# Performance work log

Hardware: AMD Instinct MI355X
Metric: run time of the kernel (lower is better)

The kernel has to match this reference:

```python
import jax, jax.numpy as jnp
import numpy as np

D_HID = 512
N_HEADS = 16
D_HEAD = D_HID // N_HEADS  # 32
D_FFN = 2048
B, N = 4, 1024
FACTOR = 0.5 / np.sqrt(D_HEAD)
EPS = 1e-5


def layer_norm(x, g, b):
    m = x.mean(-1, keepdims=True)
    v = ((x - m) ** 2).mean(-1, keepdims=True)
    return (x - m) / jnp.sqrt(v + EPS) * g + b


def setup_inputs() -> dict:
    key = jax.random.key(0)
    ks = jax.random.split(key, 24)
    s = 0.02
    p = lambda k, shape: jax.random.normal(k, shape, jnp.float32) * s
    inp = {
        'H': jax.random.normal(ks[0], (B, N, D_HID), jnp.float32),
        'V': jax.random.normal(ks[1], (B, N, 3, D_HID), jnp.float32),
        'D_batch': jax.random.normal(ks[2], (B, N, N), jnp.float32),
        'rbf_bias': jax.random.normal(ks[3], (B, 1, N, N), jnp.float32),
        'H_mask': jax.random.randint(ks[4], (B, N), 0, 2, jnp.int32),
        # attention sublayer params
        'g1': jnp.ones((D_HID,), jnp.float32), 'beta1': jnp.zeros((D_HID,), jnp.float32),
        'Wq': p(ks[5], (D_HID, 4 * D_HID)), 'bq': p(ks[6], (4 * D_HID,)),
        'Wk': p(ks[7], (D_HID, 4 * D_HID)), 'bk': p(ks[8], (4 * D_HID,)),
        'Wv': p(ks[9], (D_HID, D_HID)), 'bv': p(ks[10], (D_HID,)),
        'Wvv': p(ks[11], (D_HID, D_HID)),
        'Wo': p(ks[12], (D_HID, D_HID)), 'bo': p(ks[13], (D_HID,)),
        'Wvo': p(ks[14], (D_HID, D_HID)),
        # GVP FFN sublayer params
        'g2': jnp.ones((D_HID,), jnp.float32), 'beta2': jnp.zeros((D_HID,), jnp.float32),
        'Wlv': p(ks[15], (D_HID, 2 * D_HID)),
        'W1': p(ks[16], (2 * D_HID, D_FFN)), 'b1f': p(ks[17], (D_FFN,)),
        'W2': p(ks[18], (D_FFN, 2 * D_HID)), 'b2f': p(ks[19], (2 * D_HID,)),
    }
    return inp


def ept_forward(H, V, D_batch, rbf_bias, H_mask, g1, beta1, Wq, bq, Wk, bk, Wv, bv,
                Wvv, Wo, bo, Wvo, g2, beta2, Wlv, W1, b1f, W2, b2f):
    b, n, d = H.shape
    # ---- attention sublayer (pre-LN on H only, residual on H and V) ----
    Hn = layer_norm(H, g1, beta1)
    Hq = (Hn @ Wq + bq).reshape(b, n, N_HEADS, 4 * D_HEAD)
    Hk = (Hn @ Wk + bk).reshape(b, n, N_HEADS, 4 * D_HEAD)
    Hv = (Hn @ Wv + bv).reshape(b, n, N_HEADS, D_HEAD)
    # vector values: [b,n,3,d] -> [b,n,heads,3*dh]
    Vv = (V @ Wvv).reshape(b, n, 3, N_HEADS, D_HEAD).transpose(0, 1, 3, 2, 4)
    Vv = Vv.reshape(b, n, N_HEADS, 3 * D_HEAD)
    V_attn = jnp.concatenate([Hv, Vv], axis=-1)  # [b,n,h,4*dh]
    bias = rbf_bias + D_batch[:, None]  # [b,1,n,n]
    keep = (H_mask != 0)[:, None, None, :]  # mask keys
    bias = jnp.where(keep, bias, -jnp.inf)
    logits = jnp.einsum('bnhd,bmhd->bhnm', Hq, Hk) * FACTOR + bias
    attn = jax.nn.softmax(logits, axis=-1)
    res = jnp.einsum('bhnm,bmhd->bnhd', attn, V_attn)  # [b,n,h,4*dh]
    H_res = res[..., :D_HEAD].reshape(b, n, d)
    V_res = res[..., D_HEAD:].reshape(b, n, N_HEADS, 3, D_HEAD)
    V_res = V_res.transpose(0, 1, 3, 2, 4).reshape(b, n, 3, d)
    H = H + H_res @ Wo + bo
    V = V + V_res @ Wvo
    # ---- GVP FFN sublayer (pre-LN on H only, residual) ----
    Hn2 = layer_norm(H, g2, beta2)
    Vp = V @ Wlv  # [b,n,3,2d]
    V1, V2 = Vp[..., :d], Vp[..., d:]
    scaler = jnp.concatenate([Hn2, jnp.sqrt((V1 ** 2).sum(axis=-2))], axis=-1)
    h = jax.nn.silu(scaler @ W1 + b1f) @ W2 + b2f  # [b,n,2d]
    H = H + h[..., :d]
    V = V + h[..., None, d:] * V2
    return H, V


def reference(H, V, D_batch, rbf_bias, H_mask, g1, beta1, Wq, bq, Wk, bk, Wv, bv,
              Wvv, Wo, bo, Wvo, g2, beta2, Wlv, W1, b1f, W2, b2f):
    return ept_forward(H, V, D_batch, rbf_bias, H_mask, g1, beta1, Wq, bq, Wk, bk,
                       Wv, bv, Wvv, Wo, bo, Wvo, g2, beta2, Wlv, W1, b1f, W2, b2f)
```

## Files before the change

kernel.cpp:

```cpp
#include <hip/hip_runtime.h>
#include <math.h>

#define NBATCH 4
#define NSEQ   1024
#define DHID   512
#define NHEADS 16
#define ROWS   (NBATCH*NSEQ)
#define VROWS  (ROWS*3)
#define ATT_FACTOR 0.08838834764831845f
#define LOG2E 1.4426950408889634f
#define F2 (ATT_FACTOR*LOG2E)
#define SM_SHIFT (16.0f*LOG2E)

typedef __attribute__((ext_vector_type(8))) short short8;
typedef __attribute__((ext_vector_type(4))) float floatx4;

__device__ __forceinline__ ushort f2bf(float x) {
  union { float f; unsigned u; } v; v.f = x;
  unsigned r = v.u + 0x7fff + ((v.u >> 16) & 1);
  return (ushort)(r >> 16);
}
__device__ __forceinline__ float bf2f(ushort u) {
  union { unsigned u; float f; } v; v.u = ((unsigned)u) << 16; return v.f;
}

template<int OBF>
__global__ __launch_bounds__(256) void ln_kernel(
    const float* __restrict__ x, void* __restrict__ y, int ystride,
    const float* __restrict__ g, const float* __restrict__ beta)
{
  int row = blockIdx.x;
  int t = threadIdx.x;
  const float* xr = x + (size_t)row * DHID;
  float2 v = ((const float2*)xr)[t];
  float s  = v.x + v.y;
  float ss = v.x*v.x + v.y*v.y;
  #pragma unroll
  for (int off = 32; off > 0; off >>= 1) {
    s  += __shfl_down(s, off);
    ss += __shfl_down(ss, off);
  }
  __shared__ float red[8];
  int w = t >> 6;
  if ((t & 63) == 0) { red[w*2] = s; red[w*2+1] = ss; }
  __syncthreads();
  s  = red[0] + red[2] + red[4] + red[6];
  ss = red[1] + red[3] + red[5] + red[7];
  float mean = s * (1.0f/DHID);
  float var  = ss * (1.0f/DHID) - mean*mean;
  float rstd = rsqrtf(var + 1e-5f);
  float2 gg = ((const float2*)g)[t];
  float2 bb = ((const float2*)beta)[t];
  float2 o;
  o.x = (v.x - mean) * rstd * gg.x + bb.x;
  o.y = (v.y - mean) * rstd * gg.y + bb.y;
  if constexpr (OBF) {
    ushort2 u = { f2bf(o.x), f2bf(o.y) };
    *(ushort2*)&((ushort*)y)[(size_t)row * ystride + 2*t] = u;
  } else {
    *(float2*)&((float*)y)[(size_t)row * ystride + 2*t] = o;
  }
}

struct WJobs {
  const float* src[9];
  ushort*      dst[9];
  int K[9];
  int N[9];
  int blk0[10];
};

__global__ __launch_bounds__(256) void wtrans_all_kernel(WJobs J)
{
  __shared__ float Ts[64][65];
  int bid = blockIdx.x;
  int j = 0;
  #pragma unroll
  for (int i = 1; i < 9; i++) if (bid >= J.blk0[i]) j = i;
  const float* W = J.src[j];
  ushort* Wt = J.dst[j];
  int K = J.K[j], N = J.N[j];
  int local = bid - J.blk0[j];
  int nx = N >> 6;
  int bx = local - (local / nx) * nx;
  int by = local / nx;
  int k0 = by*64, n0 = bx*64;
  int t = threadIdx.x;
  #pragma unroll
  for (int p = 0; p < 4; p++) {
    int f = p*256 + t;
    int r = f >> 4, c = (f & 15)*4;
    float4 v = *(const float4*)&W[(size_t)(k0+r)*N + n0 + c];
    Ts[r][c] = v.x; Ts[r][c+1] = v.y; Ts[r][c+2] = v.z; Ts[r][c+3] = v.w;
  }
  __syncthreads();
  #pragma unroll
  for (int p = 0; p < 2; p++) {
    int gidx = p*256 + t;
    int nr = gidx >> 3, kc = (gidx & 7)*8;
    ushort u[8];
    #pragma unroll
    for (int x = 0; x < 8; x++) u[x] = f2bf(Ts[kc+x][nr]);
    ushort4 a = {u[0],u[1],u[2],u[3]}, b4 = {u[4],u[5],u[6],u[7]};
    *(ushort4*)&Wt[(size_t)(n0+nr)*K + k0 + kc]     = a;
    *(ushort4*)&Wt[(size_t)(n0+nr)*K + k0 + kc + 4] = b4;
  }
}

__global__ __launch_bounds__(256) void conv_bf16_kernel(
    const float* __restrict__ x, ushort* __restrict__ y)
{
  int i = blockIdx.x*256 + threadIdx.x;
  float4 v = ((const float4*)x)[i];
  ushort4 u = { f2bf(v.x), f2bf(v.y), f2bf(v.z), f2bf(v.w) };
  ((ushort4*)y)[i] = u;
}

template<int ACT, int HAS_BIAS, int HAS_RES, int OUT_BF16, int DUAL>
__global__ __launch_bounds__(256) void gemm_mfma_kernel(
    const ushort* __restrict__ A, const ushort* __restrict__ Bt,
    const float* __restrict__ bias, const float* __restrict__ resid,
    void* __restrict__ Cv, ushort* __restrict__ C2,
    int M, int N, int K)
{
  __shared__ ushort As[128*32];
  __shared__ ushort Bs[128*32];
  int t = threadIdx.x;
  int w = t >> 6, lane = t & 63;
  int q16 = lane & 15, quad = lane >> 4;
  int m0 = blockIdx.y * 128, n0 = blockIdx.x * 128;
  int wm = (w & 1) * 64, wn = (w >> 1) * 64;

  int r0 = t >> 2;
  int c0 = (t & 3) * 8;
  const ushort* Ag = A  + (size_t)(m0 + r0) * K + c0;
  const ushort* Bg = Bt + (size_t)(n0 + r0) * K + c0;

  floatx4 acc[4][4];
  #pragma unroll
  for (int i = 0; i < 4; i++)
    #pragma unroll
    for (int j = 0; j < 4; j++) acc[i][j] = (floatx4){0.f,0.f,0.f,0.f};

  for (int k0 = 0; k0 < K; k0 += 32) {
    float4 av0 = *(const float4*)(Ag + k0);
    float4 av1 = *(const float4*)(Ag + (size_t)64*K + k0);
    float4 bv0 = *(const float4*)(Bg + k0);
    float4 bv1 = *(const float4*)(Bg + (size_t)64*K + k0);
    __syncthreads();
    *(float4*)&As[r0*32 + c0]        = av0;
    *(float4*)&As[(r0 + 64)*32 + c0] = av1;
    *(float4*)&Bs[r0*32 + c0]        = bv0;
    *(float4*)&Bs[(r0 + 64)*32 + c0] = bv1;
    __syncthreads();
    short8 af[4], bf[4];
    #pragma unroll
    for (int i = 0; i < 4; i++) {
      af[i] = *(const short8*)&As[(wm + i*16 + q16)*32 + quad*8];
      bf[i] = *(const short8*)&Bs[(wn + i*16 + q16)*32 + quad*8];
    }
    #pragma unroll
    for (int i = 0; i < 4; i++)
      #pragma unroll
      for (int j = 0; j < 4; j++)
        acc[i][j] = __builtin_amdgcn_mfma_f32_16x16x32_bf16(af[i], bf[j], acc[i][j], 0, 0, 0);
  }

  float* Cf = (float*)Cv;
  ushort* Cu = (ushort*)Cv;
  float bj[4];
  #pragma unroll
  for (int j = 0; j < 4; j++)
    bj[j] = HAS_BIAS ? bias[n0 + wn + j*16 + q16] : 0.f;
  #pragma unroll
  for (int i = 0; i < 4; i++) {
    #pragma unroll
    for (int r = 0; r < 4; r++) {
      int row = m0 + wm + i*16 + quad*4 + r;
      size_t base = (size_t)row * N;
      #pragma unroll
      for (int j = 0; j < 4; j++) {
        int col = n0 + wn + j*16 + q16;
        float v = acc[i][j][r] + bj[j];
        if constexpr (ACT == 1) v = v / (1.f + __expf(-v));
        if constexpr (HAS_RES) v += resid[base + col];
        if constexpr (OUT_BF16) Cu[base + col] = f2bf(v);
        else                    Cf[base + col] = v;
        if constexpr (DUAL) C2[base + col] = f2bf(v);
      }
    }
  }
}

__global__ __launch_bounds__(256) void bias2_kernel(
    const float* __restrict__ Db, const float* __restrict__ Rb,
    const int* __restrict__ Mask, ushort* __restrict__ Bc2)
{
  int i2 = blockIdx.x*256 + threadIdx.x;
  int e = i2 * 2;
  int b = e >> 20;
  int m = e & 1023;
  float2 d = *(const float2*)&Db[e];
  float2 r = *(const float2*)&Rb[e];
  ushort2 o;
  o.x = Mask[b*NSEQ + m]     ? f2bf((d.x + r.x)*LOG2E) : f2bf(-1e30f);
  o.y = Mask[b*NSEQ + m + 1] ? f2bf((d.y + r.y)*LOG2E) : f2bf(-1e30f);
  *(ushort2*)&Bc2[e] = o;
}

__global__ __launch_bounds__(256) void vtrans_kernel(
    const float* __restrict__ Hv, const float* __restrict__ Vvr, ushort* __restrict__ Vt)
{
  __shared__ float Ts[64][33];
  int t = threadIdx.x;
  int bh = blockIdx.z;
  int b = bh >> 4, h = bh & 15;
  int dt = blockIdx.y;
  int nt = blockIdx.x;
  int d0 = dt*32, n0 = nt*64;
  #pragma unroll
  for (int i = 0; i < 2; i++) {
    int nl = (t >> 3) + i*32;
    int c4 = (t & 7)*4;
    const float* src;
    if (dt == 0) src = &Hv[(size_t)(b*NSEQ + n0 + nl)*512 + h*32 + c4];
    else { int c = dt - 1; src = &Vvr[((size_t)(b*NSEQ + n0 + nl)*3 + c)*512 + h*32 + c4]; }
    float4 v = *(const float4*)src;
    Ts[nl][c4] = v.x; Ts[nl][c4+1] = v.y; Ts[nl][c4+2] = v.z; Ts[nl][c4+3] = v.w;
  }
  __syncthreads();
  int dl = t >> 3;
  int n8 = (t & 7)*8;
  ushort u[8];
  #pragma unroll
  for (int k = 0; k < 8; k++) u[k] = f2bf(Ts[n8+k][dl]);
  size_t ob = ((size_t)bh*128 + d0 + dl)*NSEQ + n0 + n8;
  ushort4 u0 = {u[0],u[1],u[2],u[3]}, u1 = {u[4],u[5],u[6],u[7]};
  *(ushort4*)&Vt[ob]     = u0;
  *(ushort4*)&Vt[ob + 4] = u1;
}

__global__ __launch_bounds__(256) void attn_mfma_kernel(
    const ushort* __restrict__ Q, const ushort* __restrict__ K,
    const ushort* __restrict__ Vt, const ushort* __restrict__ Bc2,
    ushort* __restrict__ HRES, ushort* __restrict__ VRES)
{
  __shared__ union {
    ushort q[64][136];
    struct { ushort k[32][136]; ushort v[128][40]; } kv;
  } S;
  __shared__ ushort Ps[4][16][40];

  int t = threadIdx.x;
  int w = t >> 6, lane = t & 63;
  int q16 = lane & 15, quad = lane >> 4;
  int h = blockIdx.x, qt = blockIdx.y, b = blockIdx.z;
  int q0 = qt * 64;

  #pragma unroll
  for (int i = 0; i < 4; i++) {
    int f = t + i*256;
    int r = f >> 4, c8 = f & 15;
    *(float4*)&S.q[r][c8*8] =
        *(const float4*)&Q[(size_t)(b*NSEQ + q0 + r)*2048 + h*128 + c8*8];
  }
  __syncthreads();
  short8 qf[4];
  #pragma unroll
  for (int c = 0; c < 4; c++)
    qf[c] = *(const short8*)&S.q[w*16 + q16][c*32 + quad*8];

  floatx4 o[8];
  #pragma unroll
  for (int i = 0; i < 8; i++) o[i] = (floatx4){0.f,0.f,0.f,0.f};
  float l_i[4] = {0.f,0.f,0.f,0.f};
  const ushort* bias_base = Bc2 + (size_t)(b*NSEQ + q0 + w*16)*NSEQ;

  for (int m0 = 0; m0 < NSEQ; m0 += 32) {
    __syncthreads();
    #pragma unroll
    for (int i = 0; i < 2; i++) {
      int f = t + i*256;
      int r = f >> 4, c8 = f & 15;
      *(float4*)&S.kv.k[r][c8*8] =
          *(const float4*)&K[(size_t)(b*NSEQ + m0 + r)*2048 + h*128 + c8*8];
    }
    #pragma unroll
    for (int i = 0; i < 2; i++) {
      int f = t + i*256;
      int d = f >> 2, g = f & 3;
      *(float4*)&S.kv.v[d][g*8] =
          *(const float4*)&Vt[((size_t)(b*NHEADS + h)*128 + d)*NSEQ + m0 + g*8];
    }
    __syncthreads();

    floatx4 s0 = (floatx4){0.f,0.f,0.f,0.f};
    floatx4 s1 = (floatx4){0.f,0.f,0.f,0.f};
    #pragma unroll
    for (int c = 0; c < 4; c++) {
      short8 k0 = *(const short8*)&S.kv.k[q16][c*32 + quad*8];
      short8 k1 = *(const short8*)&S.kv.k[q16 + 16][c*32 + quad*8];
      s0 = __builtin_amdgcn_mfma_f32_16x16x32_bf16(qf[c], k0, s0, 0, 0, 0);
      s1 = __builtin_amdgcn_mfma_f32_16x16x32_bf16(qf[c], k1, s1, 0, 0, 0);
    }
    #pragma unroll
    for (int i = 0; i < 4; i++) {
      int row = quad*4 + i;
      const ushort* bp = bias_base + (size_t)row*NSEQ + m0 + q16;
      float v0 = s0[i]*F2 + bf2f(bp[0]);
      float v1 = s1[i]*F2 + bf2f(bp[16]);
      float p0 = exp2f(v0 - SM_SHIFT);
      float p1 = exp2f(v1 - SM_SHIFT);
      Ps[w][row][q16]      = f2bf(p0);
      Ps[w][row][16 + q16] = f2bf(p1);
      l_i[i] += p0 + p1;
    }
    short8 pf = *(const short8*)&Ps[w][q16][quad*8];
    #pragma unroll
    for (int tt = 0; tt < 8; tt++) {
      short8 vf = *(const short8*)&S.kv.v[tt*16 + q16][quad*8];
      o[tt] = __builtin_amdgcn_mfma_f32_16x16x32_bf16(pf, vf, o[tt], 0, 0, 0);
    }
  }
  #pragma unroll
  for (int i = 0; i < 4; i++) {
    float l = l_i[i];
    l += __shfl_xor(l, 1); l += __shfl_xor(l, 2);
    l += __shfl_xor(l, 4); l += __shfl_xor(l, 8);
    float inv = 1.0f / l;
    int grow = b*NSEQ + q0 + w*16 + quad*4 + i;
    #pragma unroll
    for (int tt = 0; tt < 2; tt++)
      HRES[(size_t)grow*512 + h*32 + tt*16 + q16] = f2bf(o[tt][i] * inv);
    #pragma unroll
    for (int tt = 2; tt < 8; tt++) {
      int c = (tt - 2) >> 1;
      int jj = ((tt - 2) & 1)*16 + q16;
      VRES[((size_t)grow*3 + c)*512 + h*32 + jj] = f2bf(o[tt][i] * inv);
    }
  }
}

__global__ __launch_bounds__(256) void vnorm_kernel(
    const float* __restrict__ VP, ushort* __restrict__ SC)
{
  int idx = blockIdx.x*256 + threadIdx.x;
  int row = idx >> 9;
  int d = idx & 511;
  const float* p = VP + (size_t)row*3072 + d;
  float a = p[0], b = p[1024], c = p[2048];
  SC[(size_t)row*1024 + 512 + d] = f2bf(sqrtf(a*a + b*b + c*c));
}

__global__ __launch_bounds__(256) void finale_kernel(
    const float* __restrict__ HH, const float* __restrict__ VP,
    float* __restrict__ Hout, float* __restrict__ Vout)
{
  int idx = blockIdx.x*256 + threadIdx.x;
  if (idx < ROWS*DHID) {
    int row = idx >> 9;
    int d = idx & 511;
    Hout[idx] += HH[(size_t)row*1024 + d];
  } else {
    int k = idx - ROWS*DHID;
    int r3 = k >> 9;
    int d = k & 511;
    int row = r3 / 3;
    Vout[k] += HH[(size_t)row*1024 + 512 + d] * VP[(size_t)r3*1024 + 512 + d];
  }
}

extern "C" void kernel_launch(void* const* d_in, const int* in_sizes, int n_in,
                              void* d_out, int out_size, void* d_ws, size_t ws_size,
                              hipStream_t stream)
{
  const float* H    = (const float*)d_in[0];
  const float* V    = (const float*)d_in[1];
  const float* Db   = (const float*)d_in[2];
  const float* Rb   = (const float*)d_in[3];
  const int*   Mask = (const int*)d_in[4];
  const float* g1   = (const float*)d_in[5];
  const float* be1  = (const float*)d_in[6];
  const float* Wq   = (const float*)d_in[7];
  const float* bq   = (const float*)d_in[8];
  const float* Wk   = (const float*)d_in[9];
  const float* bkk  = (const float*)d_in[10];
  const float* Wv   = (const float*)d_in[11];
  const float* bv   = (const float*)d_in[12];
  const float* Wvv  = (const float*)d_in[13];
  const float* Wo   = (const float*)d_in[14];
  const float* bo   = (const float*)d_in[15];
  const float* Wvo  = (const float*)d_in[16];
  const float* g2   = (const float*)d_in[17];
  const float* be2  = (const float*)d_in[18];
  const float* Wlv  = (const float*)d_in[19];
  const float* W1   = (const float*)d_in[20];
  const float* b1f  = (const float*)d_in[21];
  const float* W2   = (const float*)d_in[22];
  const float* b2f  = (const float*)d_in[23];

  float* Hout = (float*)d_out;
  float* Vout = Hout + (size_t)ROWS*DHID;

  char* w = (char*)d_ws;
  const size_t MB = 1024*1024;
  const size_t KB = 1024;
  ushort* WqT  = (ushort*)(w + 0);
  ushort* WkT  = (ushort*)(w + 2048*KB);
  ushort* WvT  = (ushort*)(w + 4096*KB);
  ushort* WvvT = (ushort*)(w + 4608*KB);
  ushort* WoT  = (ushort*)(w + 5120*KB);
  ushort* WvoT = (ushort*)(w + 5632*KB);
  ushort* WlvT = (ushort*)(w + 6144*KB);
  ushort* W1T  = (ushort*)(w + 7168*KB);
  ushort* W2T  = (ushort*)(w + 11264*KB);
  ushort* HNbf = (ushort*)(w + 16*MB);
  ushort* Qbf  = (ushort*)(w + 20*MB);
  ushort* Kbf  = (ushort*)(w + 36*MB);
  float*  HVt  = (float*)(w + 52*MB);
  float*  VVr  = (float*)(w + 60*MB);
  ushort* Vbf  = (ushort*)(w + 84*MB);
  ushort* Vtb  = (ushort*)(w + 96*MB);
  ushort* Bc2  = (ushort*)(w + 112*MB);
  ushort* HRESbf = (ushort*)(w + 120*MB);
  ushort* VRESbf = (ushort*)(w + 124*MB);
  ushort* Voutbf = (ushort*)(w + 52*MB);
  float*  VP     = (float*)(w + 64*MB);
  ushort* SCbf   = (ushort*)(w + 112*MB);
  ushort* S1bf   = (ushort*)(w + 120*MB);
  float*  HHb    = (float*)(w + 16*MB);

  dim3 blk(256);

  WJobs J;
  const float* ws_[9] = {Wq, Wk, Wv, Wvv, Wo, Wvo, Wlv, W1, W2};
  ushort* wd_[9] = {WqT, WkT, WvT, WvvT, WoT, WvoT, WlvT, W1T, W2T};
  int wk_[9] = {512, 512, 512, 512, 512, 512, 512, 1024, 2048};
  int wn_[9] = {2048, 2048, 512, 512, 512, 512, 1024, 2048, 1024};
  int off = 0;
  for (int i = 0; i < 9; i++) {
    J.src[i] = ws_[i]; J.dst[i] = wd_[i]; J.K[i] = wk_[i]; J.N[i] = wn_[i];
    J.blk0[i] = off;
    off += (wn_[i] >> 6) * (wk_[i] >> 6);
  }
  J.blk0[9] = off;
  wtrans_all_kernel<<<off, blk, 0, stream>>>(J);

  ln_kernel<1><<<ROWS, blk, 0, stream>>>(H, HNbf, DHID, g1, be1);
  conv_bf16_kernel<<<(VROWS*DHID/4)/256, blk, 0, stream>>>(V, Vbf);

  gemm_mfma_kernel<0,1,0,1,0><<<dim3(16, 32), blk, 0, stream>>>(HNbf, WqT, bq,  nullptr, Qbf, nullptr, 4096, 2048, 512);
  gemm_mfma_kernel<0,1,0,1,0><<<dim3(16, 32), blk, 0, stream>>>(HNbf, WkT, bkk, nullptr, Kbf, nullptr, 4096, 2048, 512);
  gemm_mfma_kernel<0,1,0,0,0><<<dim3( 4, 32), blk, 0, stream>>>(HNbf, WvT, bv,  nullptr, HVt, nullptr, 4096, 512, 512);
  gemm_mfma_kernel<0,0,0,0,0><<<dim3( 4, 96), blk, 0, stream>>>(Vbf, WvvT, nullptr, nullptr, VVr, nullptr, 12288, 512, 512);

  bias2_kernel<<<(NBATCH*NSEQ*NSEQ/2)/256, blk, 0, stream>>>(Db, Rb, Mask, Bc2);
  vtrans_kernel<<<dim3(16, 4, 64), blk, 0, stream>>>(HVt, VVr, Vtb);

  attn_mfma_kernel<<<dim3(16, 16, 4), blk, 0, stream>>>(Qbf, Kbf, Vtb, Bc2, HRESbf, VRESbf);

  gemm_mfma_kernel<0,1,1,0,0><<<dim3(4, 32), blk, 0, stream>>>(HRESbf, WoT,  bo, H, Hout, nullptr, 4096, 512, 512);
  gemm_mfma_kernel<0,0,1,0,1><<<dim3(4, 96), blk, 0, stream>>>(VRESbf, WvoT, nullptr, V, Vout, Voutbf, 12288, 512, 512);

  ln_kernel<1><<<ROWS, blk, 0, stream>>>(Hout, SCbf, 1024, g2, be2);
  gemm_mfma_kernel<0,0,0,0,0><<<dim3(8, 96), blk, 0, stream>>>(Voutbf, WlvT, nullptr, nullptr, VP, nullptr, 12288, 1024, 512);
  vnorm_kernel<<<(ROWS*DHID)/256, blk, 0, stream>>>(VP, SCbf);

  gemm_mfma_kernel<1,1,0,1,0><<<dim3(16, 32), blk, 0, stream>>>(SCbf, W1T, b1f, nullptr, S1bf, nullptr, 4096, 2048, 1024);
  gemm_mfma_kernel<0,1,0,0,0><<<dim3( 8, 32), blk, 0, stream>>>(S1bf, W2T, b2f, nullptr, HHb, nullptr, 4096, 1024, 2048);

  finale_kernel<<<((ROWS + VROWS)*DHID)/256, blk, 0, stream>>>(HHb, VP, Hout, Vout);
}
```

Before: 516.1 us.

## Use async LDS loads in GEMM, bf16 intermediates, fuse finale into W2 GEMM

The GEMM mainloop now uses global_load_lds to copy tiles straight into shared memory instead of staging them through registers. The Hv, Vv and VP intermediates are stored as bf16 instead of fp32, which cuts their memory traffic and lets vtrans skip its conversions. The separate finale kernel is folded into the W2 GEMM epilogue, which adds the H residual and the V gating product in place. SiLU now uses exp2f. The trade-off is lower precision in the intermediates and a strided, scattered epilogue for the V update.

```diff
diff --git a/kernel.cpp b/kernel.cpp
--- a/kernel.cpp
+++ b/kernel.cpp
@@ -22,6 +22,12 @@
 }
 __device__ __forceinline__ float bf2f(ushort u) {
   union { unsigned u; float f; } v; v.u = ((unsigned)u) << 16; return v.f;
+}
+
+__device__ __forceinline__ void async_lds16(const void* g, void* l) {
+  __builtin_amdgcn_global_load_lds(
+      (__attribute__((address_space(1))) void*)g,
+      (__attribute__((address_space(3))) void*)l, 16, 0, 0);
 }
 
 template<int OBF>
@@ -116,7 +122,7 @@
   ((ushort4*)y)[i] = u;
 }
 
-template<int ACT, int HAS_BIAS, int HAS_RES, int OUT_BF16, int DUAL>
+template<int ACT, int HAS_BIAS, int HAS_RES, int OUT_BF16, int DUAL, int FINALE>
 __global__ __launch_bounds__(256) void gemm_mfma_kernel(
     const ushort* __restrict__ A, const ushort* __restrict__ Bt,
     const float* __restrict__ bias, const float* __restrict__ resid,
@@ -143,15 +149,11 @@
     for (int j = 0; j < 4; j++) acc[i][j] = (floatx4){0.f,0.f,0.f,0.f};
 
   for (int k0 = 0; k0 < K; k0 += 32) {
-    float4 av0 = *(const float4*)(Ag + k0);
-    float4 av1 = *(const float4*)(Ag + (size_t)64*K + k0);
-    float4 bv0 = *(const float4*)(Bg + k0);
-    float4 bv1 = *(const float4*)(Bg + (size_t)64*K + k0);
     __syncthreads();
-    *(float4*)&As[r0*32 + c0]        = av0;
-    *(float4*)&As[(r0 + 64)*32 + c0] = av1;
-    *(float4*)&Bs[r0*32 + c0]        = bv0;
-    *(float4*)&Bs[(r0 + 64)*32 + c0] = bv1;
+    async_lds16(Ag + k0,                 &As[8*t]);
+    async_lds16(Ag + (size_t)64*K + k0,  &As[64*32 + 8*t]);
+    async_lds16(Bg + k0,                 &Bs[8*t]);
+    async_lds16(Bg + (size_t)64*K + k0,  &Bs[64*32 + 8*t]);
     __syncthreads();
     short8 af[4], bf[4];
     #pragma unroll
@@ -182,11 +184,25 @@
       for (int j = 0; j < 4; j++) {
         int col = n0 + wn + j*16 + q16;
         float v = acc[i][j][r] + bj[j];
-        if constexpr (ACT == 1) v = v / (1.f + __expf(-v));
-        if constexpr (HAS_RES) v += resid[base + col];
-        if constexpr (OUT_BF16) Cu[base + col] = f2bf(v);
-        else                    Cf[base + col] = v;
-        if constexpr (DUAL) C2[base + col] = f2bf(v);
+        if constexpr (ACT == 1) v = v / (1.f + exp2f(-v*LOG2E));
+        if constexpr (FINALE) {
+          if (col < 512) {
+            Cf[(size_t)row*512 + col] += v;
+          } else {
+            int d = col - 512;
+            float* Vo = const_cast<float*>(resid);
+            #pragma unroll
+            for (int c = 0; c < 3; c++) {
+              size_t r3 = (size_t)row*3 + c;
+              Vo[r3*512 + d] += v * bf2f(C2[r3*1024 + 512 + d]);
+            }
+          }
+        } else {
+          if constexpr (HAS_RES) v += resid[base + col];
+          if constexpr (OUT_BF16) Cu[base + col] = f2bf(v);
+          else                    Cf[base + col] = v;
+          if constexpr (DUAL) C2[base + col] = f2bf(v);
+        }
       }
     }
   }
@@ -209,9 +225,9 @@
 }
 
 __global__ __launch_bounds__(256) void vtrans_kernel(
-    const float* __restrict__ Hv, const float* __restrict__ Vvr, ushort* __restrict__ Vt)
-{
-  __shared__ float Ts[64][33];
+    const ushort* __restrict__ Hv, const ushort* __restrict__ Vvr, ushort* __restrict__ Vt)
+{
+  __shared__ ushort Ts[64][36];
   int t = threadIdx.x;
   int bh = blockIdx.z;
   int b = bh >> 4, h = bh & 15;
@@ -222,10 +238,10 @@
   for (int i = 0; i < 2; i++) {
     int nl = (t >> 3) + i*32;
     int c4 = (t & 7)*4;
-    const float* src;
+    const ushort* src;
     if (dt == 0) src = &Hv[(size_t)(b*NSEQ + n0 + nl)*512 + h*32 + c4];
     else { int c = dt - 1; src = &Vvr[((size_t)(b*NSEQ + n0 + nl)*3 + c)*512 + h*32 + c4]; }
-    float4 v = *(const float4*)src;
+    ushort4 v = *(const ushort4*)src;
     Ts[nl][c4] = v.x; Ts[nl][c4+1] = v.y; Ts[nl][c4+2] = v.z; Ts[nl][c4+3] = v.w;
   }
   __syncthreads();
@@ -233,7 +249,7 @@
   int n8 = (t & 7)*8;
   ushort u[8];
   #pragma unroll
-  for (int k = 0; k < 8; k++) u[k] = f2bf(Ts[n8+k][dl]);
+  for (int k = 0; k < 8; k++) u[k] = Ts[n8+k][dl];
   size_t ob = ((size_t)bh*128 + d0 + dl)*NSEQ + n0 + n8;
   ushort4 u0 = {u[0],u[1],u[2],u[3]}, u1 = {u[4],u[5],u[6],u[7]};
   *(ushort4*)&Vt[ob]     = u0;
@@ -342,32 +358,14 @@
 }
 
 __global__ __launch_bounds__(256) void vnorm_kernel(
-    const float* __restrict__ VP, ushort* __restrict__ SC)
+    const ushort* __restrict__ VP, ushort* __restrict__ SC)
 {
   int idx = blockIdx.x*256 + threadIdx.x;
   int row = idx >> 9;
   int d = idx & 511;
-  const float* p = VP + (size_t)row*3072 + d;
-  float a = p[0], b = p[1024], c = p[2048];
+  const ushort* p = VP + (size_t)row*3072 + d;
+  float a = bf2f(p[0]), b = bf2f(p[1024]), c = bf2f(p[2048]);
   SC[(size_t)row*1024 + 512 + d] = f2bf(sqrtf(a*a + b*b + c*c));
-}
-
-__global__ __launch_bounds__(256) void finale_kernel(
-    const float* __restrict__ HH, const float* __restrict__ VP,
-    float* __restrict__ Hout, float* __restrict__ Vout)
-{
-  int idx = blockIdx.x*256 + threadIdx.x;
-  if (idx < ROWS*DHID) {
-    int row = idx >> 9;
-    int d = idx & 511;
-    Hout[idx] += HH[(size_t)row*1024 + d];
-  } else {
-    int k = idx - ROWS*DHID;
-    int r3 = k >> 9;
-    int d = k & 511;
-    int row = r3 / 3;
-    Vout[k] += HH[(size_t)row*1024 + 512 + d] * VP[(size_t)r3*1024 + 512 + d];
-  }
 }
 
 extern "C" void kernel_launch(void* const* d_in, const int* in_sizes, int n_in,
@@ -414,21 +412,20 @@
   ushort* WlvT = (ushort*)(w + 6144*KB);
   ushort* W1T  = (ushort*)(w + 7168*KB);
   ushort* W2T  = (ushort*)(w + 11264*KB);
-  ushort* HNbf = (ushort*)(w + 16*MB);
-  ushort* Qbf  = (ushort*)(w + 20*MB);
-  ushort* Kbf  = (ushort*)(w + 36*MB);
-  float*  HVt  = (float*)(w + 52*MB);
-  float*  VVr  = (float*)(w + 60*MB);
-  ushort* Vbf  = (ushort*)(w + 84*MB);
-  ushort* Vtb  = (ushort*)(w + 96*MB);
-  ushort* Bc2  = (ushort*)(w + 112*MB);
-  ushort* HRESbf = (ushort*)(w + 120*MB);
-  ushort* VRESbf = (ushort*)(w + 124*MB);
+  ushort* HNbf  = (ushort*)(w + 16*MB);
+  ushort* Qbf   = (ushort*)(w + 20*MB);
+  ushort* Kbf   = (ushort*)(w + 36*MB);
+  ushort* HVtbf = (ushort*)(w + 52*MB);
+  ushort* VVrbf = (ushort*)(w + 56*MB);
+  ushort* Vbf   = (ushort*)(w + 68*MB);
+  ushort* Vtb   = (ushort*)(w + 80*MB);
+  ushort* Bc2   = (ushort*)(w + 96*MB);
+  ushort* HRESbf = (ushort*)(w + 104*MB);
+  ushort* VRESbf = (ushort*)(w + 108*MB);
   ushort* Voutbf = (ushort*)(w + 52*MB);
-  float*  VP     = (float*)(w + 64*MB);
-  ushort* SCbf   = (ushort*)(w + 112*MB);
-  ushort* S1bf   = (ushort*)(w + 120*MB);
-  float*  HHb    = (float*)(w + 16*MB);
+  ushort* VPbf   = (ushort*)(w + 64*MB);
+  ushort* SCbf   = (ushort*)(w + 96*MB);
+  ushort* S1bf   = (ushort*)(w + 104*MB);
 
   dim3 blk(256);
 
@@ -449,25 +446,23 @@
   ln_kernel<1><<<ROWS, blk, 0, stream>>>(H, HNbf, DHID, g1, be1);
   conv_bf16_kernel<<<(VROWS*DHID/4)/256, blk, 0, stream>>>(V, Vbf);
 
-  gemm_mfma_kernel<0,1,0,1,0><<<dim3(16, 32), blk, 0, stream>>>(HNbf, WqT, bq,  nullptr, Qbf, nullptr, 4096, 2048, 512);
-  gemm_mfma_kernel<0,1,0,1,0><<<dim3(16, 32), blk, 0, stream>>>(HNbf, WkT, bkk, nullptr, Kbf, nullptr, 4096, 2048, 512);
-  gemm_mfma_kernel<0,1,0,0,0><<<dim3( 4, 32), blk, 0, stream>>>(HNbf, WvT, bv,  nullptr, HVt, nullptr, 4096, 512, 512);
-  gemm_mfma_kernel<0,0,0,0,0><<<dim3( 4, 96), blk, 0, stream>>>(Vbf, WvvT, nullptr, nullptr, VVr, nullptr, 12288, 512, 512);
+  gemm_mfma_kernel<0,1,0,1,0,0><<<dim3(16, 32), blk, 0, stream>>>(HNbf, WqT, bq,  nullptr, Qbf, nullptr, 4096, 2048, 512);
+  gemm_mfma_kernel<0,1,0,1,0,0><<<dim3(16, 32), blk, 0, stream>>>(HNbf, WkT, bkk, nullptr, Kbf, nullptr, 4096, 2048, 512);
+  gemm_mfma_kernel<0,1,0,1,0,0><<<dim3( 4, 32), blk, 0, stream>>>(HNbf, WvT, bv,  nullptr, HVtbf, nullptr, 4096, 512, 512);
+  gemm_mfma_kernel<0,0,0,1,0,0><<<dim3( 4, 96), blk, 0, stream>>>(Vbf, WvvT, nullptr, nullptr, VVrbf, nullptr, 12288, 512, 512);
 
   bias2_kernel<<<(NBATCH*NSEQ*NSEQ/2)/256, blk, 0, stream>>>(Db, Rb, Mask, Bc2);
-  vtrans_kernel<<<dim3(16, 4, 64), blk, 0, stream>>>(HVt, VVr, Vtb);
+  vtrans_kernel<<<dim3(16, 4, 64), blk, 0, stream>>>(HVtbf, VVrbf, Vtb);
 
   attn_mfma_kernel<<<dim3(16, 16, 4), blk, 0, stream>>>(Qbf, Kbf, Vtb, Bc2, HRESbf, VRESbf);
 
-  gemm_mfma_kernel<0,1,1,0,0><<<dim3(4, 32), blk, 0, stream>>>(HRESbf, WoT,  bo, H, Hout, nullptr, 4096, 512, 512);
-  gemm_mfma_kernel<0,0,1,0,1><<<dim3(4, 96), blk, 0, stream>>>(VRESbf, WvoT, nullptr, V, Vout, Voutbf, 12288, 512, 512);
+  gemm_mfma_kernel<0,1,1,0,0,0><<<dim3(4, 32), blk, 0, stream>>>(HRESbf, WoT,  bo, H, Hout, nullptr, 4096, 512, 512);
+  gemm_mfma_kernel<0,0,1,0,1,0><<<dim3(4, 96), blk, 0, stream>>>(VRESbf, WvoT, nullptr, V, Vout, Voutbf, 12288, 512, 512);
 
   ln_kernel<1><<<ROWS, blk, 0, stream>>>(Hout, SCbf, 1024, g2, be2);
-  gemm_mfma_kernel<0,0,0,0,0><<<dim3(8, 96), blk, 0, stream>>>(Voutbf, WlvT, nullptr, nullptr, VP, nullptr, 12288, 1024, 512);
-  vnorm_kernel<<<(ROWS*DHID)/256, blk, 0, stream>>>(VP, SCbf);
-
-  gemm_mfma_kernel<1,1,0,1,0><<<dim3(16, 32), blk, 0, stream>>>(SCbf, W1T, b1f, nullptr, S1bf, nullptr, 4096, 2048, 1024);
-  gemm_mfma_kernel<0,1,0,0,0><<<dim3( 8, 32), blk, 0, stream>>>(S1bf, W2T, b2f, nullptr, HHb, nullptr, 4096, 1024, 2048);
-
-  finale_kernel<<<((ROWS + VROWS)*DHID)/256, blk, 0, stream>>>(HHb, VP, Hout, Vout);
-}
+  gemm_mfma_kernel<0,0,0,1,0,0><<<dim3(8, 96), blk, 0, stream>>>(Voutbf, WlvT, nullptr, nullptr, VPbf, nullptr, 12288, 1024, 512);
+  vnorm_kernel<<<(ROWS*DHID)/256, blk, 0, stream>>>(VPbf, SCbf);
+
+  gemm_mfma_kernel<1,1,0,1,0,0><<<dim3(16, 32), blk, 0, stream>>>(SCbf, W1T, b1f, nullptr, S1bf, nullptr, 4096, 2048, 1024);
+  gemm_mfma_kernel<0,1,0,0,0,1><<<dim3( 8, 32), blk, 0, stream>>>(S1bf, W2T, b2f, Vout, Hout, VPbf, 4096, 1024, 2048);
+}
```

Measured after the change: 527.6 us. 1.02x slower.
